# Optimization experiments

Hardware: AMD Instinct MI355X
Metric: run time of the kernel (lower is better)

The kernel has to match this reference:

```python
import jax, jax.numpy as jnp
import numpy as np

B, L, DIM, DFF = 4, 2048, 1024, 4096
EPS = 1e-5

def setup_inputs() -> dict:
    key = jax.random.key(0)
    ks = jax.random.split(key, 10)
    s = 0.02
    return {
        "x": jax.random.normal(ks[0], (B, L, DIM), dtype=jnp.float32),
        "ln_g": jnp.ones((DIM,), jnp.float32),
        "ln_b": jnp.zeros((DIM,), jnp.float32),
        "phazor": jax.random.normal(ks[1], (DIM, 2), dtype=jnp.float32),
        "phazor_init": jax.random.normal(ks[2], (DIM, 2), dtype=jnp.float32),
        "w1": jax.random.normal(ks[3], (DIM, DFF), dtype=jnp.float32) * s,
        "b1": jnp.zeros((DFF,), jnp.float32),
        "w2": jax.random.normal(ks[4], (DFF, DIM), dtype=jnp.float32) * s,
        "b2": jnp.zeros((DIM,), jnp.float32),
        "last_conv_re": jax.random.normal(ks[5], (B, DIM), dtype=jnp.float32),
        "last_conv_im": jax.random.normal(ks[6], (B, DIM), dtype=jnp.float32),
    }

def layer_norm(x, g, b):
    mu = jnp.mean(x, axis=-1, keepdims=True)
    var = jnp.var(x, axis=-1, keepdims=True)
    return (x - mu) * jax.lax.rsqrt(var + EPS) * g + b

def spiral_conv(x, phazor, phazor_init, last_re, last_im):
    # x: [B, L, D] float32
    Lx = x.shape[1]
    p = jax.lax.complex(phazor[:, 0], phazor[:, 1])          # [D]
    p_init = jax.lax.complex(phazor_init[:, 0], phazor_init[:, 1])
    pa = jnp.abs(p)
    p = p / pa * jnp.exp(-pa)                                 # normalized decay phazor
    t = jnp.arange(Lx)
    prog = p[None, :] ** t[:, None]                           # [L, D] p^t
    filt = prog * p_init[None, :]                             # [L, D]
    ffilt = jnp.fft.fft(filt, n=2 * Lx, axis=0)               # [2L, D]
    xf = jnp.fft.fft(x.astype(jnp.complex64), n=2 * Lx, axis=1)  # [B, 2L, D]
    conv = jnp.fft.ifft(ffilt[None] * xf, axis=1)[:, :Lx]     # [B, L, D]
    last = jax.lax.complex(last_re, last_im)                  # [B, D] (detached state)
    conv_with_past = conv + last[:, None, :] * prog[None] * p[None, None, :]
    return conv_with_past.real

def reference(x, ln_g, ln_b, phazor, phazor_init, w1, b1, w2, b2, last_conv_re, last_conv_im):
    x_ = x
    h = layer_norm(x, ln_g, ln_b)
    h = spiral_conv(h, phazor, phazor_init, last_conv_re, last_conv_im)
    x = h + x_
    x_ = x
    h = layer_norm(x, ln_g, ln_b)  # same LayerNorm params reused, as in the source
    h = jax.nn.silu(h @ w1 + b1) @ w2 + b2  # FFN, dropout=0 (eval)
    return h + x_

if __name__ == "__main__":
    out = reference(**setup_inputs())
    print(out.shape, out.dtype)
```

## Files before the change

kernel.cpp:

```cpp
#include <hip/hip_runtime.h>
#include <stdint.h>
#include <stddef.h>

#define DIMC 1024
#define LSEQ 2048
#define BSZ  4
#define DFFC 4096
#define NTOK (BSZ*LSEQ)
#define NCHUNK 32
#define CHUNK 64

typedef __bf16 bf16x8 __attribute__((ext_vector_type(8)));
typedef float  f32x4  __attribute__((ext_vector_type(4)));

__device__ __forceinline__ unsigned short f2bf(float f) {
  unsigned int u = __float_as_uint(f);
  u += 0x7fffu + ((u >> 16) & 1u);
  return (unsigned short)(u >> 16);
}

__device__ __forceinline__ void async16(const void* g, void* l) {
  __builtin_amdgcn_global_load_lds(
      (const __attribute__((address_space(1))) unsigned int*)(uintptr_t)g,
      (__attribute__((address_space(3))) unsigned int*)(uintptr_t)l,
      16, 0, 0);
}

__device__ __forceinline__ void bar() {
  asm volatile("" ::: "memory");
  __builtin_amdgcn_s_barrier();
  asm volatile("" ::: "memory");
}
#define LGKM0 do { asm volatile("s_waitcnt lgkmcnt(0)" ::: "memory"); \
                   __builtin_amdgcn_sched_barrier(0); } while (0)
#define VMCNT(n) asm volatile("s_waitcnt vmcnt(" #n ")" ::: "memory")
#define MFMA_BF16 __builtin_amdgcn_mfma_f32_16x16x32_bf16

__global__ __launch_bounds__(256) void ln_stats(const float* __restrict__ x,
                                                float* __restrict__ mu,
                                                float* __restrict__ rstd) {
  const int token = blockIdx.x;
  const float4* xp = (const float4*)(x + (size_t)token * DIMC);
  float4 v = xp[threadIdx.x];
  float s  = v.x + v.y + v.z + v.w;
  float s2 = v.x*v.x + v.y*v.y + v.z*v.z + v.w*v.w;
  #pragma unroll
  for (int o = 32; o; o >>= 1) { s += __shfl_down(s, o); s2 += __shfl_down(s2, o); }
  __shared__ float sh[8];
  const int lane = threadIdx.x & 63, w = threadIdx.x >> 6;
  if (lane == 0) { sh[w] = s; sh[4 + w] = s2; }
  __syncthreads();
  if (threadIdx.x == 0) {
    float ts  = sh[0] + sh[1] + sh[2] + sh[3];
    float ts2 = sh[4] + sh[5] + sh[6] + sh[7];
    float m = ts * (1.f / DIMC);
    float var = ts2 * (1.f / DIMC) - m * m;
    mu[token] = m;
    rstd[token] = rsqrtf(var + 1e-5f);
  }
}

__global__ __launch_bounds__(256) void ln_apply_bf16(const float* __restrict__ x,
                                                     const float* __restrict__ mu,
                                                     const float* __restrict__ rstd,
                                                     const float* __restrict__ g,
                                                     const float* __restrict__ bb,
                                                     unsigned short* __restrict__ out) {
  const size_t i = (size_t)blockIdx.x * 256 + threadIdx.x;
  float4 v = ((const float4*)x)[i];
  const int token = (int)(i >> 8);
  const int d4 = (int)(i & 255);
  float4 gv = ((const float4*)g)[d4];
  float4 bv = ((const float4*)bb)[d4];
  const float m = mu[token], r = rstd[token];
  ushort4 o;
  o.x = f2bf((v.x - m) * r * gv.x + bv.x);
  o.y = f2bf((v.y - m) * r * gv.y + bv.y);
  o.z = f2bf((v.z - m) * r * gv.z + bv.z);
  o.w = f2bf((v.w - m) * r * gv.w + bv.w);
  ((ushort4*)out)[i] = o;
}

__global__ __launch_bounds__(256) void transpose_bf16(const float* __restrict__ w,
                                                      unsigned short* __restrict__ wt,
                                                      int K, int N) {
  __shared__ float tile[32][33];
  const int n0 = blockIdx.x * 32, k0 = blockIdx.y * 32;
  const int tx = threadIdx.x, ty = threadIdx.y;
  #pragma unroll
  for (int i = 0; i < 32; i += 8)
    tile[ty + i][tx] = w[(size_t)(k0 + ty + i) * N + n0 + tx];
  __syncthreads();
  #pragma unroll
  for (int i = 0; i < 32; i += 8)
    wt[(size_t)(n0 + ty + i) * K + k0 + tx] = f2bf(tile[tx][ty + i]);
}

__device__ __forceinline__ void get_p(const float* __restrict__ phazor, int d,
                                      float& p_re, float& p_im) {
  float pre = phazor[2 * d], pim = phazor[2 * d + 1];
  float a = sqrtf(pre * pre + pim * pim);
  float sc = expf(-a) / a;
  p_re = pre * sc;
  p_im = pim * sc;
}

__global__ __launch_bounds__(256) void scan_phase1(const float* __restrict__ x,
                                                   const float* __restrict__ mu,
                                                   const float* __restrict__ rstd,
                                                   const float* __restrict__ g,
                                                   const float* __restrict__ bb,
                                                   const float* __restrict__ phazor,
                                                   float* __restrict__ Sre,
                                                   float* __restrict__ Sim) {
  const int d = blockIdx.x * 256 + threadIdx.x;
  const int c = blockIdx.y;
  const int b = blockIdx.z;
  float p_re, p_im; get_p(phazor, d, p_re, p_im);
  const float gd = g[d], bd = bb[d];
  const int t0 = c * CHUNK;
  const float* xp  = x + ((size_t)(b * LSEQ + t0)) * DIMC + d;
  const float* mup = mu + b * LSEQ + t0;
  const float* rp  = rstd + b * LSEQ + t0;
  float r_re = 0.f, r_im = 0.f;
  #pragma unroll 4
  for (int s = 0; s < CHUNK; ++s) {
    float hv = (xp[(size_t)s * DIMC] - mup[s]) * rp[s] * gd + bd;
    float nr = p_re * r_re - p_im * r_im + hv;
    float ni = p_re * r_im + p_im * r_re;
    r_re = nr; r_im = ni;
  }
  const int bd_i = b * DIMC + d;
  Sre[c * (BSZ * DIMC) + bd_i] = r_re;
  Sim[c * (BSZ * DIMC) + bd_i] = r_im;
}

__global__ __launch_bounds__(256) void scan_phase2(const float* __restrict__ phazor,
                                                   const float* __restrict__ Sre,
                                                   const float* __restrict__ Sim,
                                                   float* __restrict__ Cre,
                                                   float* __restrict__ Cim) {
  const int bd = blockIdx.x * 256 + threadIdx.x;
  const int d = bd & (DIMC - 1);
  float p_re, p_im; get_p(phazor, d, p_re, p_im);
  float br = p_re, bi = p_im;
  #pragma unroll
  for (int i = 0; i < 6; ++i) { float t = br * br - bi * bi; bi = 2.f * br * bi; br = t; }
  float R_re = 0.f, R_im = 0.f;
  for (int c = 0; c < NCHUNK; ++c) {
    Cre[c * (BSZ * DIMC) + bd] = R_re;
    Cim[c * (BSZ * DIMC) + bd] = R_im;
    float sre = Sre[c * (BSZ * DIMC) + bd], sim = Sim[c * (BSZ * DIMC) + bd];
    float nr = br * R_re - bi * R_im + sre;
    float ni = br * R_im + bi * R_re + sim;
    R_re = nr; R_im = ni;
  }
}

__global__ __launch_bounds__(256) void scan_phase3(const float* __restrict__ x,
                                                   const float* __restrict__ mu,
                                                   const float* __restrict__ rstd,
                                                   const float* __restrict__ g,
                                                   const float* __restrict__ bb,
                                                   const float* __restrict__ phazor,
                                                   const float* __restrict__ phazor_init,
                                                   const float* __restrict__ last_re,
                                                   const float* __restrict__ last_im,
                                                   const float* __restrict__ Cre,
                                                   const float* __restrict__ Cim,
                                                   float* __restrict__ x2) {
  const int d = blockIdx.x * 256 + threadIdx.x;
  const int c = blockIdx.y;
  const int b = blockIdx.z;
  float p_re, p_im; get_p(phazor, d, p_re, p_im);
  const float pi_re = phazor_init[2 * d], pi_im = phazor_init[2 * d + 1];
  const float gd = g[d], bd_ = bb[d];
  const int bd_i = b * DIMC + d;
  float r_re = Cre[c * (BSZ * DIMC) + bd_i];
  float r_im = Cim[c * (BSZ * DIMC) + bd_i];
  float br = p_re, bi = p_im;
  #pragma unroll
  for (int i = 0; i < 6; ++i) { float t = br * br - bi * bi; bi = 2.f * br * bi; br = t; }
  float er = 1.f, ei = 0.f;
  int e = c;
  while (e) {
    if (e & 1) { float t = er * br - ei * bi; ei = er * bi + ei * br; er = t; }
    float t2 = br * br - bi * bi; bi = 2.f * br * bi; br = t2;
    e >>= 1;
  }
  const float lre = last_re[bd_i], lim = last_im[bd_i];
  float q_re = lre * er - lim * ei;
  float q_im = lre * ei + lim * er;
  const int t0 = c * CHUNK;
  const float* xp  = x + ((size_t)(b * LSEQ + t0)) * DIMC + d;
  const float* mup = mu + b * LSEQ + t0;
  const float* rp  = rstd + b * LSEQ + t0;
  float* op = x2 + ((size_t)(b * LSEQ + t0)) * DIMC + d;
  #pragma unroll 4
  for (int s = 0; s < CHUNK; ++s) {
    float xv = xp[(size_t)s * DIMC];
    float hv = (xv - mup[s]) * rp[s] * gd + bd_;
    float nr = p_re * r_re - p_im * r_im + hv;
    float ni = p_re * r_im + p_im * r_re;
    r_re = nr; r_im = ni;
    float nq = p_re * q_re - p_im * q_im;
    q_im = p_re * q_im + p_im * q_re;
    q_re = nq;
    op[(size_t)s * DIMC] = pi_re * r_re - pi_im * r_im + q_re + xv;
  }
}

template<int BN, int EPI>
__global__ __launch_bounds__(512, 2) void gemm8(const unsigned short* __restrict__ A,
                                                const unsigned short* __restrict__ Bt,
                                                const float* __restrict__ bias,
                                                const float* __restrict__ resid,
                                                void* __restrict__ outp,
                                                int M, int N, int K) {
  constexpr int AUS = 256 * 32;
  constexpr int BUS = BN * 32;
  constexpr int BUFUS = 2 * AUS + 2 * BUS;
  constexpr int NI = BN / 64;
  __shared__ __align__(16) unsigned short lds[2 * BUFUS];

  const int tid  = threadIdx.x;
  const int lane = tid & 63;
  const int wave = tid >> 6;
  const int wm = (wave & 1) * 128;
  const int wn = (wave >> 1) * (BN / 4);
  const int r15 = lane & 15;
  const int cus = ((lane >> 4) ^ ((r15 >> 1) & 3)) * 8;

  int bid = blockIdx.x;
  const int cpx = gridDim.x >> 3;
  bid = (bid & 7) * cpx + (bid >> 3);
  const int ntn = N / BN;
  const int tm = (bid / ntn) * 256;
  const int tn = (bid % ntn) * BN;
  const int NT = K >> 6;

  f32x4 acc[8][NI];
  #pragma unroll
  for (int i = 0; i < 8; ++i)
    #pragma unroll
    for (int j = 0; j < NI; ++j) acc[i][j] = (f32x4){0.f, 0.f, 0.f, 0.f};

  auto stageA = [&](int buf, int kk, int k0) {
    unsigned short* blk = lds + buf * BUFUS + kk * AUS;
    const unsigned short* g = A + (size_t)tm * K + k0 + kk * 32;
    #pragma unroll
    for (int r = 0; r < 2; ++r) {
      const int s = r * 512 + tid;
      const int row = s >> 2;
      const int cg = (s & 3) ^ ((s >> 3) & 3);
      async16(g + (size_t)row * K + cg * 8, blk + (size_t)s * 8);
    }
  };
  auto stageB = [&](int buf, int kk, int k0) {
    unsigned short* blk = lds + buf * BUFUS + 2 * AUS + kk * BUS;
    const unsigned short* g = Bt + (size_t)tn * K + k0 + kk * 32;
    #pragma unroll
    for (int r = 0; r < BN / 128; ++r) {
      const int s = r * 512 + tid;
      const int row = s >> 2;
      const int cg = (s & 3) ^ ((s >> 3) & 3);
      async16(g + (size_t)row * K + cg * 8, blk + (size_t)s * 8);
    }
  };
  auto rdA = [&](int buf, int kk, int mi) -> bf16x8 {
    return *(const bf16x8*)(lds + buf * BUFUS + kk * AUS + (wm + mi * 16 + r15) * 32 + cus);
  };
  auto rdB = [&](int buf, int kk, int ni) -> bf16x8 {
    return *(const bf16x8*)(lds + buf * BUFUS + 2 * AUS + kk * BUS + (wn + ni * 16 + r15) * 32 + cus);
  };

  bf16x8 af[8], bq0, bq1;

  stageA(0, 0, 0); stageB(0, 0, 0); stageA(0, 1, 0); stageB(0, 1, 0);
  if constexpr (BN == 256) VMCNT(4); else VMCNT(3);
  bar();

  for (int t = 0; t < NT - 1; ++t) {
    const int buf = t & 1, nb = buf ^ 1, kn = (t + 1) << 6;
    if constexpr (BN == 256) {
      #pragma unroll
      for (int mi = 0; mi < 8; ++mi) af[mi] = rdA(buf, 0, mi);
      bq0 = rdB(buf, 0, 0); bq1 = rdB(buf, 0, 1);
      stageA(nb, 0, kn);
      bar(); LGKM0;
      __builtin_amdgcn_s_setprio(1);
      #pragma unroll
      for (int mi = 0; mi < 8; ++mi) {
        acc[mi][0] = MFMA_BF16(af[mi], bq0, acc[mi][0], 0, 0, 0);
        acc[mi][1] = MFMA_BF16(af[mi], bq1, acc[mi][1], 0, 0, 0);
      }
      __builtin_amdgcn_s_setprio(0);
      bar();
      bq0 = rdB(buf, 0, 2); bq1 = rdB(buf, 0, 3);
      stageB(nb, 0, kn);
      bar(); LGKM0;
      __builtin_amdgcn_s_setprio(1);
      #pragma unroll
      for (int mi = 0; mi < 8; ++mi) {
        acc[mi][2] = MFMA_BF16(af[mi], bq0, acc[mi][2], 0, 0, 0);
        acc[mi][3] = MFMA_BF16(af[mi], bq1, acc[mi][3], 0, 0, 0);
      }
      __builtin_amdgcn_s_setprio(0);
      VMCNT(4);
      bar();
      #pragma unroll
      for (int mi = 0; mi < 8; ++mi) af[mi] = rdA(buf, 1, mi);
      bq0 = rdB(buf, 1, 0); bq1 = rdB(buf, 1, 1);
      stageA(nb, 1, kn);
      bar(); LGKM0;
      __builtin_amdgcn_s_setprio(1);
      #pragma unroll
      for (int mi = 0; mi < 8; ++mi) {
        acc[mi][0] = MFMA_BF16(af[mi], bq0, acc[mi][0], 0, 0, 0);
        acc[mi][1] = MFMA_BF16(af[mi], bq1, acc[mi][1], 0, 0, 0);
      }
      __builtin_amdgcn_s_setprio(0);
      bar();
      bq0 = rdB(buf, 1, 2); bq1 = rdB(buf, 1, 3);
      stageB(nb, 1, kn);
      bar(); LGKM0;
      __builtin_amdgcn_s_setprio(1);
      #pragma unroll
      for (int mi = 0; mi < 8; ++mi) {
        acc[mi][2] = MFMA_BF16(af[mi], bq0, acc[mi][2], 0, 0, 0);
        acc[mi][3] = MFMA_BF16(af[mi], bq1, acc[mi][3], 0, 0, 0);
      }
      __builtin_amdgcn_s_setprio(0);
      VMCNT(4);
      bar();
    } else {
      #pragma unroll
      for (int mi = 0; mi < 8; ++mi) af[mi] = rdA(buf, 0, mi);
      bq0 = rdB(buf, 0, 0); bq1 = rdB(buf, 0, 1);
      stageA(nb, 0, kn); stageB(nb, 0, kn);
      bar(); LGKM0;
      __builtin_amdgcn_s_setprio(1);
      #pragma unroll
      for (int mi = 0; mi < 8; ++mi) {
        acc[mi][0] = MFMA_BF16(af[mi], bq0, acc[mi][0], 0, 0, 0);
        acc[mi][1] = MFMA_BF16(af[mi], bq1, acc[mi][1], 0, 0, 0);
      }
      __builtin_amdgcn_s_setprio(0);
      VMCNT(3);
      bar();
      #pragma unroll
      for (int mi = 0; mi < 8; ++mi) af[mi] = rdA(buf, 1, mi);
      bq0 = rdB(buf, 1, 0); bq1 = rdB(buf, 1, 1);
      stageA(nb, 1, kn); stageB(nb, 1, kn);
      bar(); LGKM0;
      __builtin_amdgcn_s_setprio(1);
      #pragma unroll
      for (int mi = 0; mi < 8; ++mi) {
        acc[mi][0] = MFMA_BF16(af[mi], bq0, acc[mi][0], 0, 0, 0);
        acc[mi][1] = MFMA_BF16(af[mi], bq1, acc[mi][1], 0, 0, 0);
      }
      __builtin_amdgcn_s_setprio(0);
      VMCNT(3);
      bar();
    }
  }

  {
    const int buf = (NT - 1) & 1;
    if constexpr (BN == 256) {
      #pragma unroll
      for (int mi = 0; mi < 8; ++mi) af[mi] = rdA(buf, 0, mi);
      bq0 = rdB(buf, 0, 0); bq1 = rdB(buf, 0, 1);
      bar(); LGKM0;
      #pragma unroll
      for (int mi = 0; mi < 8; ++mi) {
        acc[mi][0] = MFMA_BF16(af[mi], bq0, acc[mi][0], 0, 0, 0);
        acc[mi][1] = MFMA_BF16(af[mi], bq1, acc[mi][1], 0, 0, 0);
      }
      bar();
      bq0 = rdB(buf, 0, 2); bq1 = rdB(buf, 0, 3);
      bar(); LGKM0;
      #pragma unroll
      for (int mi = 0; mi < 8; ++mi) {
        acc[mi][2] = MFMA_BF16(af[mi], bq0, acc[mi][2], 0, 0, 0);
        acc[mi][3] = MFMA_BF16(af[mi], bq1, acc[mi][3], 0, 0, 0);
      }
      VMCNT(0);
      bar();
      #pragma unroll
      for (int mi = 0; mi < 8; ++mi) af[mi] = rdA(buf, 1, mi);
      bq0 = rdB(buf, 1, 0); bq1 = rdB(buf, 1, 1);
      bar(); LGKM0;
      #pragma unroll
      for (int mi = 0; mi < 8; ++mi) {
        acc[mi][0] = MFMA_BF16(af[mi], bq0, acc[mi][0], 0, 0, 0);
        acc[mi][1] = MFMA_BF16(af[mi], bq1, acc[mi][1], 0, 0, 0);
      }
      bar();
      bq0 = rdB(buf, 1, 2); bq1 = rdB(buf, 1, 3);
      LGKM0;
      #pragma unroll
      for (int mi = 0; mi < 8; ++mi) {
        acc[mi][2] = MFMA_BF16(af[mi], bq0, acc[mi][2], 0, 0, 0);
        acc[mi][3] = MFMA_BF16(af[mi], bq1, acc[mi][3], 0, 0, 0);
      }
    } else {
      #pragma unroll
      for (int mi = 0; mi < 8; ++mi) af[mi] = rdA(buf, 0, mi);
      bq0 = rdB(buf, 0, 0); bq1 = rdB(buf, 0, 1);
      bar(); LGKM0;
      #pragma unroll
      for (int mi = 0; mi < 8; ++mi) {
        acc[mi][0] = MFMA_BF16(af[mi], bq0, acc[mi][0], 0, 0, 0);
        acc[mi][1] = MFMA_BF16(af[mi], bq1, acc[mi][1], 0, 0, 0);
      }
      VMCNT(0);
      bar();
      #pragma unroll
      for (int mi = 0; mi < 8; ++mi) af[mi] = rdA(buf, 1, mi);
      bq0 = rdB(buf, 1, 0); bq1 = rdB(buf, 1, 1);
      LGKM0;
      #pragma unroll
      for (int mi = 0; mi < 8; ++mi) {
        acc[mi][0] = MFMA_BF16(af[mi], bq0, acc[mi][0], 0, 0, 0);
        acc[mi][1] = MFMA_BF16(af[mi], bq1, acc[mi][1], 0, 0, 0);
      }
    }
  }

  const int rg = (lane >> 4) * 4;
  #pragma unroll
  for (int ni = 0; ni < NI; ++ni) {
    const int n = tn + wn + ni * 16 + r15;
    const float bv = bias[n];
    #pragma unroll
    for (int mi = 0; mi < 8; ++mi) {
      const int rb = tm + wm + mi * 16 + rg;
      #pragma unroll
      for (int j = 0; j < 4; ++j) {
        float v = acc[mi][ni][j] + bv;
        if constexpr (EPI == 0) {
          v = v / (1.f + __expf(-v));
          ((unsigned short*)outp)[(size_t)(rb + j) * N + n] = f2bf(v);
        } else {
          v += resid[(size_t)(rb + j) * N + n];
          ((float*)outp)[(size_t)(rb + j) * N + n] = v;
        }
      }
    }
  }
}

extern "C" void kernel_launch(void* const* d_in, const int* in_sizes, int n_in,
                              void* d_out, int out_size, void* d_ws, size_t ws_size,
                              hipStream_t stream) {
  const float* x           = (const float*)d_in[0];
  const float* ln_g        = (const float*)d_in[1];
  const float* ln_b        = (const float*)d_in[2];
  const float* phazor      = (const float*)d_in[3];
  const float* phazor_init = (const float*)d_in[4];
  const float* w1          = (const float*)d_in[5];
  const float* b1          = (const float*)d_in[6];
  const float* w2          = (const float*)d_in[7];
  const float* b2          = (const float*)d_in[8];
  const float* last_re     = (const float*)d_in[9];
  const float* last_im     = (const float*)d_in[10];
  float* out = (float*)d_out;
  char* ws = (char*)d_ws;
  const size_t MB = 1ull << 20;

  float* x2  = (float*)(ws);
  float* mu1 = (float*)(ws + 32 * MB);
  float* rs1 = (float*)(ws + 32 * MB + 64 * 1024);
  float* mu2 = (float*)(ws + 32 * MB + 128 * 1024);
  float* rs2 = (float*)(ws + 32 * MB + 192 * 1024);
  float* Sre = (float*)(ws + 32 * MB + 256 * 1024);
  float* Sim = (float*)(ws + 32 * MB + 768 * 1024);
  float* Cre = (float*)(ws + 32 * MB + 1280 * 1024);
  float* Cim = (float*)(ws + 32 * MB + 1792 * 1024);
  unsigned short* h2  = (unsigned short*)(ws + 35 * MB);
  unsigned short* hid = (unsigned short*)(ws + 51 * MB);
  unsigned short* w1t = (unsigned short*)(ws + 115 * MB);
  unsigned short* w2t = (unsigned short*)(ws + 123 * MB);

  transpose_bf16<<<dim3(DFFC / 32, DIMC / 32), dim3(32, 8), 0, stream>>>(w1, w1t, DIMC, DFFC);
  transpose_bf16<<<dim3(DIMC / 32, DFFC / 32), dim3(32, 8), 0, stream>>>(w2, w2t, DFFC, DIMC);

  ln_stats<<<NTOK, 256, 0, stream>>>(x, mu1, rs1);
  scan_phase1<<<dim3(DIMC / 256, NCHUNK, BSZ), 256, 0, stream>>>(x, mu1, rs1, ln_g, ln_b, phazor, Sre, Sim);
  scan_phase2<<<(BSZ * DIMC) / 256, 256, 0, stream>>>(phazor, Sre, Sim, Cre, Cim);
  scan_phase3<<<dim3(DIMC / 256, NCHUNK, BSZ), 256, 0, stream>>>(x, mu1, rs1, ln_g, ln_b, phazor,
                                                                 phazor_init, last_re, last_im,
                                                                 Cre, Cim, x2);
  ln_stats<<<NTOK, 256, 0, stream>>>(x2, mu2, rs2);
  ln_apply_bf16<<<NTOK, 256, 0, stream>>>(x2, mu2, rs2, ln_g, ln_b, h2);

  gemm8<256, 0><<<(NTOK / 256) * (DFFC / 256), 512, 0, stream>>>(h2, w1t, b1, nullptr, hid,
                                                                 NTOK, DFFC, DIMC);
  gemm8<128, 1><<<(NTOK / 256) * (DIMC / 128), 512, 0, stream>>>(hid, w2t, b2, x2, out,
                                                                 NTOK, DIMC, DFFC);
}
```

Baseline: 329.3 us.

## Fuse second LayerNorm, restage GEMM epilogue through LDS, retile BN=128 waves

Merges the second LayerNorm's stats and apply kernels into one kernel, so x2 is read once instead of twice and one launch disappears. The GEMM epilogue now writes results to swizzled LDS and then issues coalesced 16-byte global stores and residual loads, replacing scattered scalar stores. The BN=128 GEMM changes its wave layout from 128x32 to 64x64 per wave and now runs the same four-phase loop as BN=256. The explicit lgkmcnt waits and sched barriers are removed, which leaves LDS-read ordering to the compiler and could cost correctness or scheduling quality.

```diff
diff --git a/kernel.cpp b/kernel.cpp
--- a/kernel.cpp
+++ b/kernel.cpp
@@ -31,8 +31,6 @@
   __builtin_amdgcn_s_barrier();
   asm volatile("" ::: "memory");
 }
-#define LGKM0 do { asm volatile("s_waitcnt lgkmcnt(0)" ::: "memory"); \
-                   __builtin_amdgcn_sched_barrier(0); } while (0)
 #define VMCNT(n) asm volatile("s_waitcnt vmcnt(" #n ")" ::: "memory")
 #define MFMA_BF16 __builtin_amdgcn_mfma_f32_16x16x32_bf16
 
@@ -60,25 +58,39 @@
   }
 }
 
-__global__ __launch_bounds__(256) void ln_apply_bf16(const float* __restrict__ x,
-                                                     const float* __restrict__ mu,
-                                                     const float* __restrict__ rstd,
+__global__ __launch_bounds__(256) void ln_fused_bf16(const float* __restrict__ x,
                                                      const float* __restrict__ g,
                                                      const float* __restrict__ bb,
                                                      unsigned short* __restrict__ out) {
-  const size_t i = (size_t)blockIdx.x * 256 + threadIdx.x;
-  float4 v = ((const float4*)x)[i];
-  const int token = (int)(i >> 8);
-  const int d4 = (int)(i & 255);
-  float4 gv = ((const float4*)g)[d4];
-  float4 bv = ((const float4*)bb)[d4];
-  const float m = mu[token], r = rstd[token];
+  const int token = blockIdx.x;
+  const float4* xp = (const float4*)(x + (size_t)token * DIMC);
+  float4 v = xp[threadIdx.x];
+  float s  = v.x + v.y + v.z + v.w;
+  float s2 = v.x*v.x + v.y*v.y + v.z*v.z + v.w*v.w;
+  #pragma unroll
+  for (int o = 32; o; o >>= 1) { s += __shfl_down(s, o); s2 += __shfl_down(s2, o); }
+  __shared__ float sh[10];
+  const int lane = threadIdx.x & 63, w = threadIdx.x >> 6;
+  if (lane == 0) { sh[w] = s; sh[4 + w] = s2; }
+  __syncthreads();
+  if (threadIdx.x == 0) {
+    float ts  = sh[0] + sh[1] + sh[2] + sh[3];
+    float ts2 = sh[4] + sh[5] + sh[6] + sh[7];
+    float m = ts * (1.f / DIMC);
+    float var = ts2 * (1.f / DIMC) - m * m;
+    sh[8] = m;
+    sh[9] = rsqrtf(var + 1e-5f);
+  }
+  __syncthreads();
+  const float m = sh[8], r = sh[9];
+  float4 gv = ((const float4*)g)[threadIdx.x];
+  float4 bv = ((const float4*)bb)[threadIdx.x];
   ushort4 o;
   o.x = f2bf((v.x - m) * r * gv.x + bv.x);
   o.y = f2bf((v.y - m) * r * gv.y + bv.y);
   o.z = f2bf((v.z - m) * r * gv.z + bv.z);
   o.w = f2bf((v.w - m) * r * gv.w + bv.w);
-  ((ushort4*)out)[i] = o;
+  ((ushort4*)(out + (size_t)token * DIMC))[threadIdx.x] = o;
 }
 
 __global__ __launch_bounds__(256) void transpose_bf16(const float* __restrict__ w,
@@ -220,14 +232,15 @@
   constexpr int AUS = 256 * 32;
   constexpr int BUS = BN * 32;
   constexpr int BUFUS = 2 * AUS + 2 * BUS;
-  constexpr int NI = BN / 64;
-  __shared__ __align__(16) unsigned short lds[2 * BUFUS];
+  constexpr int MI = (BN == 256) ? 8 : 4;
+  constexpr int LDSUS = (2 * BUFUS > 65536) ? 2 * BUFUS : 65536;
+  __shared__ __align__(16) unsigned short lds[LDSUS];
 
   const int tid  = threadIdx.x;
   const int lane = tid & 63;
   const int wave = tid >> 6;
-  const int wm = (wave & 1) * 128;
-  const int wn = (wave >> 1) * (BN / 4);
+  const int wm = (BN == 256) ? (wave & 1) * 128 : (wave >> 1) * 64;
+  const int wn = (BN == 256) ? (wave >> 1) * 64  : (wave & 1) * 64;
   const int r15 = lane & 15;
   const int cus = ((lane >> 4) ^ ((r15 >> 1) & 3)) * 8;
 
@@ -239,11 +252,11 @@
   const int tn = (bid % ntn) * BN;
   const int NT = K >> 6;
 
-  f32x4 acc[8][NI];
-  #pragma unroll
-  for (int i = 0; i < 8; ++i)
-    #pragma unroll
-    for (int j = 0; j < NI; ++j) acc[i][j] = (f32x4){0.f, 0.f, 0.f, 0.f};
+  f32x4 acc[MI][4];
+  #pragma unroll
+  for (int i = 0; i < MI; ++i)
+    #pragma unroll
+    for (int j = 0; j < 4; ++j) acc[i][j] = (f32x4){0.f, 0.f, 0.f, 0.f};
 
   auto stageA = [&](int buf, int kk, int k0) {
     unsigned short* blk = lds + buf * BUFUS + kk * AUS;
@@ -274,7 +287,7 @@
     return *(const bf16x8*)(lds + buf * BUFUS + 2 * AUS + kk * BUS + (wn + ni * 16 + r15) * 32 + cus);
   };
 
-  bf16x8 af[8], bq0, bq1;
+  bf16x8 af[MI], bq0, bq1, bq2, bq3;
 
   stageA(0, 0, 0); stageB(0, 0, 0); stageA(0, 1, 0); stageB(0, 1, 0);
   if constexpr (BN == 256) VMCNT(4); else VMCNT(3);
@@ -282,171 +295,154 @@
 
   for (int t = 0; t < NT - 1; ++t) {
     const int buf = t & 1, nb = buf ^ 1, kn = (t + 1) << 6;
-    if constexpr (BN == 256) {
-      #pragma unroll
-      for (int mi = 0; mi < 8; ++mi) af[mi] = rdA(buf, 0, mi);
-      bq0 = rdB(buf, 0, 0); bq1 = rdB(buf, 0, 1);
-      stageA(nb, 0, kn);
-      bar(); LGKM0;
-      __builtin_amdgcn_s_setprio(1);
-      #pragma unroll
-      for (int mi = 0; mi < 8; ++mi) {
-        acc[mi][0] = MFMA_BF16(af[mi], bq0, acc[mi][0], 0, 0, 0);
-        acc[mi][1] = MFMA_BF16(af[mi], bq1, acc[mi][1], 0, 0, 0);
-      }
-      __builtin_amdgcn_s_setprio(0);
-      bar();
-      bq0 = rdB(buf, 0, 2); bq1 = rdB(buf, 0, 3);
-      stageB(nb, 0, kn);
-      bar(); LGKM0;
-      __builtin_amdgcn_s_setprio(1);
-      #pragma unroll
-      for (int mi = 0; mi < 8; ++mi) {
-        acc[mi][2] = MFMA_BF16(af[mi], bq0, acc[mi][2], 0, 0, 0);
-        acc[mi][3] = MFMA_BF16(af[mi], bq1, acc[mi][3], 0, 0, 0);
-      }
-      __builtin_amdgcn_s_setprio(0);
-      VMCNT(4);
-      bar();
-      #pragma unroll
-      for (int mi = 0; mi < 8; ++mi) af[mi] = rdA(buf, 1, mi);
-      bq0 = rdB(buf, 1, 0); bq1 = rdB(buf, 1, 1);
-      stageA(nb, 1, kn);
-      bar(); LGKM0;
-      __builtin_amdgcn_s_setprio(1);
-      #pragma unroll
-      for (int mi = 0; mi < 8; ++mi) {
-        acc[mi][0] = MFMA_BF16(af[mi], bq0, acc[mi][0], 0, 0, 0);
-        acc[mi][1] = MFMA_BF16(af[mi], bq1, acc[mi][1], 0, 0, 0);
-      }
-      __builtin_amdgcn_s_setprio(0);
-      bar();
-      bq0 = rdB(buf, 1, 2); bq1 = rdB(buf, 1, 3);
-      stageB(nb, 1, kn);
-      bar(); LGKM0;
-      __builtin_amdgcn_s_setprio(1);
-      #pragma unroll
-      for (int mi = 0; mi < 8; ++mi) {
-        acc[mi][2] = MFMA_BF16(af[mi], bq0, acc[mi][2], 0, 0, 0);
-        acc[mi][3] = MFMA_BF16(af[mi], bq1, acc[mi][3], 0, 0, 0);
-      }
-      __builtin_amdgcn_s_setprio(0);
-      VMCNT(4);
-      bar();
-    } else {
-      #pragma unroll
-      for (int mi = 0; mi < 8; ++mi) af[mi] = rdA(buf, 0, mi);
-      bq0 = rdB(buf, 0, 0); bq1 = rdB(buf, 0, 1);
-      stageA(nb, 0, kn); stageB(nb, 0, kn);
-      bar(); LGKM0;
-      __builtin_amdgcn_s_setprio(1);
-      #pragma unroll
-      for (int mi = 0; mi < 8; ++mi) {
-        acc[mi][0] = MFMA_BF16(af[mi], bq0, acc[mi][0], 0, 0, 0);
-        acc[mi][1] = MFMA_BF16(af[mi], bq1, acc[mi][1], 0, 0, 0);
-      }
-      __builtin_amdgcn_s_setprio(0);
-      VMCNT(3);
-      bar();
-      #pragma unroll
-      for (int mi = 0; mi < 8; ++mi) af[mi] = rdA(buf, 1, mi);
-      bq0 = rdB(buf, 1, 0); bq1 = rdB(buf, 1, 1);
-      stageA(nb, 1, kn); stageB(nb, 1, kn);
-      bar(); LGKM0;
-      __builtin_amdgcn_s_setprio(1);
-      #pragma unroll
-      for (int mi = 0; mi < 8; ++mi) {
-        acc[mi][0] = MFMA_BF16(af[mi], bq0, acc[mi][0], 0, 0, 0);
-        acc[mi][1] = MFMA_BF16(af[mi], bq1, acc[mi][1], 0, 0, 0);
-      }
-      __builtin_amdgcn_s_setprio(0);
-      VMCNT(3);
-      bar();
-    }
+    #pragma unroll
+    for (int mi = 0; mi < MI; ++mi) af[mi] = rdA(buf, 0, mi);
+    bq0 = rdB(buf, 0, 0); bq1 = rdB(buf, 0, 1);
+    stageA(nb, 0, kn);
+    bar();
+    __builtin_amdgcn_s_setprio(1);
+    #pragma unroll
+    for (int mi = 0; mi < MI; ++mi) {
+      acc[mi][0] = MFMA_BF16(af[mi], bq0, acc[mi][0], 0, 0, 0);
+      acc[mi][1] = MFMA_BF16(af[mi], bq1, acc[mi][1], 0, 0, 0);
+    }
+    __builtin_amdgcn_s_setprio(0);
+    bar();
+    bq2 = rdB(buf, 0, 2); bq3 = rdB(buf, 0, 3);
+    stageB(nb, 0, kn);
+    bar();
+    __builtin_amdgcn_s_setprio(1);
+    #pragma unroll
+    for (int mi = 0; mi < MI; ++mi) {
+      acc[mi][2] = MFMA_BF16(af[mi], bq2, acc[mi][2], 0, 0, 0);
+      acc[mi][3] = MFMA_BF16(af[mi], bq3, acc[mi][3], 0, 0, 0);
+    }
+    __builtin_amdgcn_s_setprio(0);
+    if constexpr (BN == 256) VMCNT(4); else VMCNT(3);
+    bar();
+    #pragma unroll
+    for (int mi = 0; mi < MI; ++mi) af[mi] = rdA(buf, 1, mi);
+    bq0 = rdB(buf, 1, 0); bq1 = rdB(buf, 1, 1);
+    stageA(nb, 1, kn);
+    bar();
+    __builtin_amdgcn_s_setprio(1);
+    #pragma unroll
+    for (int mi = 0; mi < MI; ++mi) {
+      acc[mi][0] = MFMA_BF16(af[mi], bq0, acc[mi][0], 0, 0, 0);
+      acc[mi][1] = MFMA_BF16(af[mi], bq1, acc[mi][1], 0, 0, 0);
+    }
+    __builtin_amdgcn_s_setprio(0);
+    bar();
+    bq2 = rdB(buf, 1, 2); bq3 = rdB(buf, 1, 3);
+    stageB(nb, 1, kn);
+    bar();
+    __builtin_amdgcn_s_setprio(1);
+    #pragma unroll
+    for (int mi = 0; mi < MI; ++mi) {
+      acc[mi][2] = MFMA_BF16(af[mi], bq2, acc[mi][2], 0, 0, 0);
+      acc[mi][3] = MFMA_BF16(af[mi], bq3, acc[mi][3], 0, 0, 0);
+    }
+    __builtin_amdgcn_s_setprio(0);
+    if constexpr (BN == 256) VMCNT(4); else VMCNT(3);
+    bar();
   }
 
   {
     const int buf = (NT - 1) & 1;
-    if constexpr (BN == 256) {
+    #pragma unroll
+    for (int mi = 0; mi < MI; ++mi) af[mi] = rdA(buf, 0, mi);
+    bq0 = rdB(buf, 0, 0); bq1 = rdB(buf, 0, 1);
+    bar();
+    #pragma unroll
+    for (int mi = 0; mi < MI; ++mi) {
+      acc[mi][0] = MFMA_BF16(af[mi], bq0, acc[mi][0], 0, 0, 0);
+      acc[mi][1] = MFMA_BF16(af[mi], bq1, acc[mi][1], 0, 0, 0);
+    }
+    bar();
+    bq2 = rdB(buf, 0, 2); bq3 = rdB(buf, 0, 3);
+    #pragma unroll
+    for (int mi = 0; mi < MI; ++mi) {
+      acc[mi][2] = MFMA_BF16(af[mi], bq2, acc[mi][2], 0, 0, 0);
+      acc[mi][3] = MFMA_BF16(af[mi], bq3, acc[mi][3], 0, 0, 0);
+    }
+    VMCNT(0);
+    bar();
+    #pragma unroll
+    for (int mi = 0; mi < MI; ++mi) af[mi] = rdA(buf, 1, mi);
+    bq0 = rdB(buf, 1, 0); bq1 = rdB(buf, 1, 1);
+    bar();
+    #pragma unroll
+    for (int mi = 0; mi < MI; ++mi) {
+      acc[mi][0] = MFMA_BF16(af[mi], bq0, acc[mi][0], 0, 0, 0);
+      acc[mi][1] = MFMA_BF16(af[mi], bq1, acc[mi][1], 0, 0, 0);
+    }
+    bar();
+    bq2 = rdB(buf, 1, 2); bq3 = rdB(buf, 1, 3);
+    #pragma unroll
+    for (int mi = 0; mi < MI; ++mi) {
+      acc[mi][2] = MFMA_BF16(af[mi], bq2, acc[mi][2], 0, 0, 0);
+      acc[mi][3] = MFMA_BF16(af[mi], bq3, acc[mi][3], 0, 0, 0);
+    }
+  }
+
+  const int rg = (lane >> 4) * 4;
+  float bias_r[4];
+  #pragma unroll
+  for (int ni = 0; ni < 4; ++ni) bias_r[ni] = bias[tn + wn + ni * 16 + r15];
+
+  bar();
+  if constexpr (EPI == 0) {
+    unsigned short* C = lds;
+    #pragma unroll
+    for (int mi = 0; mi < MI; ++mi)
       #pragma unroll
-      for (int mi = 0; mi < 8; ++mi) af[mi] = rdA(buf, 0, mi);
-      bq0 = rdB(buf, 0, 0); bq1 = rdB(buf, 0, 1);
-      bar(); LGKM0;
-      #pragma unroll
-      for (int mi = 0; mi < 8; ++mi) {
-        acc[mi][0] = MFMA_BF16(af[mi], bq0, acc[mi][0], 0, 0, 0);
-        acc[mi][1] = MFMA_BF16(af[mi], bq1, acc[mi][1], 0, 0, 0);
-      }
-      bar();
-      bq0 = rdB(buf, 0, 2); bq1 = rdB(buf, 0, 3);
-      bar(); LGKM0;
-      #pragma unroll
-      for (int mi = 0; mi < 8; ++mi) {
-        acc[mi][2] = MFMA_BF16(af[mi], bq0, acc[mi][2], 0, 0, 0);
-        acc[mi][3] = MFMA_BF16(af[mi], bq1, acc[mi][3], 0, 0, 0);
-      }
-      VMCNT(0);
-      bar();
-      #pragma unroll
-      for (int mi = 0; mi < 8; ++mi) af[mi] = rdA(buf, 1, mi);
-      bq0 = rdB(buf, 1, 0); bq1 = rdB(buf, 1, 1);
-      bar(); LGKM0;
-      #pragma unroll
-      for (int mi = 0; mi < 8; ++mi) {
-        acc[mi][0] = MFMA_BF16(af[mi], bq0, acc[mi][0], 0, 0, 0);
-        acc[mi][1] = MFMA_BF16(af[mi], bq1, acc[mi][1], 0, 0, 0);
-      }
-      bar();
-      bq0 = rdB(buf, 1, 2); bq1 = rdB(buf, 1, 3);
-      LGKM0;
-      #pragma unroll
-      for (int mi = 0; mi < 8; ++mi) {
-        acc[mi][2] = MFMA_BF16(af[mi], bq0, acc[mi][2], 0, 0, 0);
-        acc[mi][3] = MFMA_BF16(af[mi], bq1, acc[mi][3], 0, 0, 0);
-      }
-    } else {
-      #pragma unroll
-      for (int mi = 0; mi < 8; ++mi) af[mi] = rdA(buf, 0, mi);
-      bq0 = rdB(buf, 0, 0); bq1 = rdB(buf, 0, 1);
-      bar(); LGKM0;
-      #pragma unroll
-      for (int mi = 0; mi < 8; ++mi) {
-        acc[mi][0] = MFMA_BF16(af[mi], bq0, acc[mi][0], 0, 0, 0);
-        acc[mi][1] = MFMA_BF16(af[mi], bq1, acc[mi][1], 0, 0, 0);
-      }
-      VMCNT(0);
-      bar();
-      #pragma unroll
-      for (int mi = 0; mi < 8; ++mi) af[mi] = rdA(buf, 1, mi);
-      bq0 = rdB(buf, 1, 0); bq1 = rdB(buf, 1, 1);
-      LGKM0;
-      #pragma unroll
-      for (int mi = 0; mi < 8; ++mi) {
-        acc[mi][0] = MFMA_BF16(af[mi], bq0, acc[mi][0], 0, 0, 0);
-        acc[mi][1] = MFMA_BF16(af[mi], bq1, acc[mi][1], 0, 0, 0);
-      }
-    }
-  }
-
-  const int rg = (lane >> 4) * 4;
-  #pragma unroll
-  for (int ni = 0; ni < NI; ++ni) {
-    const int n = tn + wn + ni * 16 + r15;
-    const float bv = bias[n];
-    #pragma unroll
-    for (int mi = 0; mi < 8; ++mi) {
-      const int rb = tm + wm + mi * 16 + rg;
-      #pragma unroll
-      for (int j = 0; j < 4; ++j) {
-        float v = acc[mi][ni][j] + bv;
-        if constexpr (EPI == 0) {
+      for (int ni = 0; ni < 4; ++ni) {
+        const int c0 = wn + ni * 16 + r15;
+        #pragma unroll
+        for (int j = 0; j < 4; ++j) {
+          const int r = wm + mi * 16 + rg + j;
+          const int key = (((r & 3) ^ ((r >> 2) & 3)) << 4);
+          float v = acc[mi][ni][j] + bias_r[ni];
           v = v / (1.f + __expf(-v));
-          ((unsigned short*)outp)[(size_t)(rb + j) * N + n] = f2bf(v);
-        } else {
-          v += resid[(size_t)(rb + j) * N + n];
-          ((float*)outp)[(size_t)(rb + j) * N + n] = v;
+          C[r * 256 + (c0 ^ key)] = f2bf(v);
         }
       }
+    bar();
+    #pragma unroll
+    for (int i = 0; i < 16; ++i) {
+      const int off = i * 4096 + tid * 8;
+      const int r = off >> 8;
+      const int pc = off & 255;
+      const int key = (((r & 3) ^ ((r >> 2) & 3)) << 4);
+      bf16x8 v = *(const bf16x8*)(C + off);
+      *(bf16x8*)((unsigned short*)outp + (size_t)(tm + r) * N + tn + (pc ^ key)) = v;
+    }
+  } else {
+    float* C = (float*)lds;
+    #pragma unroll
+    for (int mi = 0; mi < MI; ++mi)
+      #pragma unroll
+      for (int ni = 0; ni < 4; ++ni) {
+        const int c0 = wn + ni * 16 + r15;
+        #pragma unroll
+        for (int j = 0; j < 4; ++j) {
+          const int r = wm + mi * 16 + rg + j;
+          const int key = (((r & 3) ^ ((r >> 2) & 3)) << 4);
+          C[r * 128 + (c0 ^ key)] = acc[mi][ni][j] + bias_r[ni];
+        }
+      }
+    bar();
+    #pragma unroll
+    for (int i = 0; i < 16; ++i) {
+      const int off = i * 2048 + tid * 4;
+      const int r = off >> 7;
+      const int pc = off & 127;
+      const int key = (((r & 3) ^ ((r >> 2) & 3)) << 4);
+      f32x4 v = *(const f32x4*)(C + off);
+      const size_t gaddr = (size_t)(tm + r) * N + tn + (pc ^ key);
+      f32x4 rv = *(const f32x4*)(resid + gaddr);
+      v += rv;
+      *(f32x4*)((float*)outp + gaddr) = v;
     }
   }
 }
@@ -472,8 +468,6 @@
   float* x2  = (float*)(ws);
   float* mu1 = (float*)(ws + 32 * MB);
   float* rs1 = (float*)(ws + 32 * MB + 64 * 1024);
-  float* mu2 = (float*)(ws + 32 * MB + 128 * 1024);
-  float* rs2 = (float*)(ws + 32 * MB + 192 * 1024);
   float* Sre = (float*)(ws + 32 * MB + 256 * 1024);
   float* Sim = (float*)(ws + 32 * MB + 768 * 1024);
   float* Cre = (float*)(ws + 32 * MB + 1280 * 1024);
@@ -492,8 +486,7 @@
   scan_phase3<<<dim3(DIMC / 256, NCHUNK, BSZ), 256, 0, stream>>>(x, mu1, rs1, ln_g, ln_b, phazor,
                                                                  phazor_init, last_re, last_im,
                                                                  Cre, Cim, x2);
-  ln_stats<<<NTOK, 256, 0, stream>>>(x2, mu2, rs2);
-  ln_apply_bf16<<<NTOK, 256, 0, stream>>>(x2, mu2, rs2, ln_g, ln_b, h2);
+  ln_fused_bf16<<<NTOK, 256, 0, stream>>>(x2, ln_g, ln_b, h2);
 
   gemm8<256, 0><<<(NTOK / 256) * (DFFC / 256), 512, 0, stream>>>(h2, w1t, b1, nullptr, hid,
                                                                  NTOK, DFFC, DIMC);
```

New measurement: 329.1 us. About the same (-0.0%).
